# Optimization experiments

Hardware: AMD Instinct MI355X
Metric: run time of the kernel (lower is better)

The kernel has to match this reference:

```python
import jax, jax.numpy as jnp
import numpy as np
import math

B, S, D = 2, 2048, 1024
H, KV, HD = 16, 4, 64
N_REP = H // KV
ROPE_THETA = 1.0e6


def _rope_tables(seq_len, head_dim, theta):
    inv_freq = 1.0 / (theta ** (np.arange(0, head_dim, 2, dtype=np.float32) / head_dim))
    t = np.arange(seq_len, dtype=np.float32)
    freqs = np.outer(t, inv_freq)                      # [S, HD/2]
    emb = np.concatenate([freqs, freqs], axis=-1)      # [S, HD]
    return jnp.asarray(np.cos(emb)), jnp.asarray(np.sin(emb))


def setup_inputs() -> dict:
    key = jax.random.key(0)
    ks = jax.random.split(key, 6)
    cos, sin = _rope_tables(S, HD, ROPE_THETA)
    scale = 0.02
    return {
        "x": jax.random.normal(ks[0], (B, S, D), dtype=jnp.float32),
        "cos": cos,
        "sin": sin,
        "Wq": jax.random.normal(ks[1], (D, H * HD), dtype=jnp.float32) * scale,
        "Wk": jax.random.normal(ks[2], (D, KV * HD), dtype=jnp.float32) * scale,
        "Wv": jax.random.normal(ks[3], (D, KV * HD), dtype=jnp.float32) * scale,
        "Wo": jax.random.normal(ks[4], (H * HD, D), dtype=jnp.float32) * scale,
    }


def _rotate_half(u):
    u1, u2 = u[..., : HD // 2], u[..., HD // 2 :]
    return jnp.concatenate([-u2, u1], axis=-1)


def reference(x, cos, sin, Wq, Wk, Wv, Wo):
    bsz, seq_len, _ = x.shape
    q = (x @ Wq).reshape(bsz, seq_len, H, HD)   # [B,S,H,HD]
    k = (x @ Wk).reshape(bsz, seq_len, KV, HD)  # [B,S,KV,HD]
    v = (x @ Wv).reshape(bsz, seq_len, KV, HD)

    # RoPE: cos/sin [S,HD] broadcast over batch and heads (unsqueeze_dim=1)
    c = cos[:seq_len][None, :, None, :]
    s = sin[:seq_len][None, :, None, :]
    q = q * c + _rotate_half(q) * s
    k = k * c + _rotate_half(k) * s

    # repeat_kv: expand KV heads groupwise to H heads
    k = jnp.repeat(k, N_REP, axis=2)  # [B,S,H,HD]
    v = jnp.repeat(v, N_REP, axis=2)

    q = q.transpose(0, 2, 1, 3)  # [B,H,S,HD]
    k = k.transpose(0, 2, 1, 3)
    v = v.transpose(0, 2, 1, 3)

    scores = jnp.einsum("bhqd,bhkd->bhqk", q, k) / math.sqrt(HD)
    causal = jnp.tril(jnp.ones((seq_len, seq_len), dtype=bool))
    scores = jnp.where(causal[None, None], scores, jnp.finfo(jnp.float32).min)
    probs = jax.nn.softmax(scores.astype(jnp.float32), axis=-1).astype(x.dtype)

    out = jnp.einsum("bhqk,bhkd->bhqd", probs, v)        # [B,H,S,HD]
    out = out.transpose(0, 2, 1, 3).reshape(bsz, seq_len, H * HD)
    return out @ Wo
```

## Files before the change

### kernel.cpp

```cpp
#include <hip/hip_runtime.h>

#define SS 2048
#define NH 16
#define NKV 4
#define HD 64

typedef __bf16 bf16;
typedef __bf16 bf16x4 __attribute__((ext_vector_type(4)));
typedef __bf16 bf16x8 __attribute__((ext_vector_type(8)));
typedef float f32x4 __attribute__((ext_vector_type(4)));

#define SM_SCALE 0.18033688011f

__device__ __forceinline__ void gl_lds16(const bf16* g, bf16* l) {
    __builtin_amdgcn_global_load_lds((const __attribute__((address_space(1))) void*)g,
                                     (__attribute__((address_space(3))) void*)l, 16, 0, 0);
}

__global__ __launch_bounds__(256) void prep_kernel(
    const float* __restrict__ x,
    const float* __restrict__ Wq, const float* __restrict__ Wk,
    const float* __restrict__ Wv, const float* __restrict__ Wo,
    bf16* __restrict__ wqkv_t, bf16* __restrict__ wo_t, bf16* __restrict__ xb)
{
    const int blk = blockIdx.x;
    const int tid = threadIdx.x;
    if (blk >= 640) {
        const size_t i0 = (size_t)(blk - 640) * 16384;
        #pragma unroll
        for (int i = 0; i < 16; ++i) {
            const size_t idx = i0 + i * 1024 + tid * 4;
            const float4 v = *(const float4*)&x[idx];
            bf16x4 o4;
            o4[0] = (bf16)v.x; o4[1] = (bf16)v.y; o4[2] = (bf16)v.z; o4[3] = (bf16)v.w;
            *(bf16x4*)&xb[idx] = o4;
        }
        return;
    }
    const float* W; bf16* Wt; int N, n0, k0;
    if (blk < 256)      { W = Wq; Wt = wqkv_t;                       N = 1024; n0 = (blk & 15) * 64;         k0 = (blk >> 4) * 64; }
    else if (blk < 320) { W = Wk; Wt = wqkv_t + (size_t)1024 * 1024; N = 256;  n0 = ((blk - 256) & 3) * 64;  k0 = ((blk - 256) >> 2) * 64; }
    else if (blk < 384) { W = Wv; Wt = wqkv_t + (size_t)1280 * 1024; N = 256;  n0 = ((blk - 320) & 3) * 64;  k0 = ((blk - 320) >> 2) * 64; }
    else                { W = Wo; Wt = wo_t;                         N = 1024; n0 = ((blk - 384) & 15) * 64; k0 = ((blk - 384) >> 4) * 64; }

    __shared__ float Ts[64][65];
    const int c = tid & 63, rr = tid >> 6;
    #pragma unroll
    for (int i = 0; i < 16; ++i) {
        const int kk = i * 4 + rr;
        Ts[kk][c] = W[(size_t)(k0 + kk) * N + n0 + c];
    }
    __syncthreads();
    #pragma unroll
    for (int i = 0; i < 16; ++i) {
        const int nn = i * 4 + rr;
        Wt[(size_t)(n0 + nn) * 1024 + k0 + c] = (bf16)Ts[c][nn];
    }
}

template<int EPI>
__global__ __launch_bounds__(256) void gemm_bt_kernel(
    const bf16* __restrict__ A, const bf16* __restrict__ Bt, float* __restrict__ C,
    const float* __restrict__ cosp, const float* __restrict__ sinp,
    bf16* __restrict__ qo, bf16* __restrict__ ko, bf16* __restrict__ vto,
    int N, int K, int CB)
{
    __shared__ bf16 As[2][128 * 64];
    __shared__ bf16 Bs[2][128 * 64];
    const int bid = blockIdx.x;
    const int j = bid >> 3;
    const int rb = (bid & 7) + 8 * (j / CB);
    const int cb = j % CB;
    const int m0 = rb * 128, n0 = cb * 128;
    const int tid = threadIdx.x;
    const int w = tid >> 6, lane = tid & 63, g = lane >> 4, li = lane & 15;
    const int wm = w >> 1, wn = w & 1;

    f32x4 acc[4][4];
    const f32x4 z = {0.f, 0.f, 0.f, 0.f};
    #pragma unroll
    for (int i = 0; i < 4; ++i)
        #pragma unroll
        for (int jj = 0; jj < 4; ++jj) acc[i][jj] = z;

    const int srow = tid >> 3;
    const int schunk = ((tid & 7) ^ (srow & 7)) * 8;
    const bf16* pA[4];
    const bf16* pB[4];
    #pragma unroll
    for (int s = 0; s < 4; ++s) {
        pA[s] = A  + (size_t)(m0 + s * 32 + srow) * K + schunk;
        pB[s] = Bt + (size_t)(n0 + s * 32 + srow) * K + schunk;
    }
    const int lw = w * 512;

    const int NT = K >> 6;

    #pragma unroll
    for (int s = 0; s < 4; ++s) gl_lds16(pA[s], &As[0][s * 2048 + lw]);
    #pragma unroll
    for (int s = 0; s < 4; ++s) gl_lds16(pB[s], &Bs[0][s * 2048 + lw]);
    __syncthreads();

    for (int t = 0; t < NT; ++t) {
        const int cur = t & 1;
        const int kk = (t + 1) << 6;
        if (t + 1 < NT) {
            #pragma unroll
            for (int s = 0; s < 4; ++s) gl_lds16(pA[s] + kk, &As[cur ^ 1][s * 2048 + lw]);
            #pragma unroll
            for (int s = 0; s < 4; ++s) gl_lds16(pB[s] + kk, &Bs[cur ^ 1][s * 2048 + lw]);
        }
        #pragma unroll
        for (int tt = 0; tt < 2; ++tt) {
            const int phys = ((tt * 4 + g) ^ (li & 7)) * 8;
            bf16x8 af[4], bfr[4];
            #pragma unroll
            for (int mi = 0; mi < 4; ++mi) af[mi] = *(const bf16x8*)&As[cur][(wm * 64 + mi * 16 + li) * 64 + phys];
            #pragma unroll
            for (int ni = 0; ni < 4; ++ni) bfr[ni] = *(const bf16x8*)&Bs[cur][(wn * 64 + ni * 16 + li) * 64 + phys];
            #pragma unroll
            for (int mi = 0; mi < 4; ++mi)
                #pragma unroll
                for (int ni = 0; ni < 4; ++ni)
                    acc[mi][ni] = __builtin_amdgcn_mfma_f32_16x16x32_bf16(af[mi], bfr[ni], acc[mi][ni], 0, 0, 0);
        }
        __syncthreads();
    }

    const int row0 = m0 + wm * 64, col0 = n0 + wn * 64;
    if (EPI == 0) {
        #pragma unroll
        for (int mi = 0; mi < 4; ++mi)
            #pragma unroll
            for (int ni = 0; ni < 4; ++ni)
                #pragma unroll
                for (int r = 0; r < 4; ++r)
                    C[(size_t)(row0 + mi * 16 + g * 4 + r) * N + col0 + ni * 16 + li] = acc[mi][ni][r];
    } else {
        #pragma unroll
        for (int ni = 0; ni < 4; ++ni) {
            const int col = col0 + ni * 16 + li;
            const int d = col & 63;
            #pragma unroll
            for (int mi = 0; mi < 4; ++mi) {
                #pragma unroll
                for (int r = 0; r < 4; ++r) {
                    const int row = row0 + mi * 16 + g * 4 + r;
                    const int bb = row >> 11, s = row & 2047;
                    float val = acc[mi][ni][r];
                    if (col < 1280) {
                        const float pairv = acc[mi][ni ^ 2][r];
                        const float rot = (d < 32) ? -pairv : pairv;
                        val = val * cosp[s * 64 + d] + rot * sinp[s * 64 + d];
                    }
                    if (col < 1024) {
                        const int hh = col >> 6;
                        qo[(((size_t)bb * NH + hh) * SS + s) * HD + d] = (bf16)(val * SM_SCALE);
                    } else if (col < 1280) {
                        const int kh = (col - 1024) >> 6;
                        ko[(((size_t)bb * NKV + kh) * SS + s) * HD + d] = (bf16)val;
                    } else {
                        const int kh = (col - 1280) >> 6;
                        vto[(((size_t)bb * NKV + kh) * HD + d) * SS + s] = (bf16)val;
                    }
                }
            }
        }
    }
}

__global__ __launch_bounds__(256) void flash_kernel(const bf16* __restrict__ q, const bf16* __restrict__ k,
                                                    const bf16* __restrict__ vt, bf16* __restrict__ o)
{
    __shared__ bf16 Ks[128 * 64];
    __shared__ bf16 Vt[64 * 128];
    __shared__ bf16 Ps[4][16 * 64];

    const int blk = blockIdx.x;
    const int qt = 31 - (blk >> 5);
    const int h = blk & 15;
    const int b = (blk >> 4) & 1;
    const int kvh = h >> 2;
    const int tid = threadIdx.x;
    const int w = tid >> 6, lane = tid & 63, g = lane >> 4, li = lane & 15;

    const bf16* qh = q + ((size_t)b * NH + h) * SS * HD;
    const bf16* kh = k + ((size_t)b * NKV + kvh) * SS * HD;
    const bf16* vh = vt + ((size_t)b * NKV + kvh) * (size_t)HD * SS;

    bf16x8 ones;
    #pragma unroll
    for (int jj = 0; jj < 8; ++jj) ones[jj] = (bf16)1.0f;
    const f32x4 z = {0.f, 0.f, 0.f, 0.f};

    const bf16* qrow = qh + (size_t)(qt * 64 + w * 16 + li) * HD;
    bf16x8 qf[2];
    qf[0] = *(const bf16x8*)(qrow + g * 8);
    qf[1] = *(const bf16x8*)(qrow + 32 + g * 8);

    const int ksrow = tid >> 3;
    const int kchunk = ((tid & 7) ^ (ksrow & 7)) * 8;
    const int vsrow = tid >> 4;
    const int vchunk = (((tid & 15) ^ (vsrow & 7)) & 15) * 8;
    bf16* lK = Ks + (size_t)w * 512;
    bf16* lV = Vt + (size_t)w * 512;

    const int xm = (li & 7) << 1;

    f32x4 o_acc[4], l_acc;
    #pragma unroll
    for (int nt = 0; nt < 4; ++nt) o_acc[nt] = z;
    l_acc = z;

    for (int kt0 = 0; kt0 <= qt; kt0 += 2) {
        __syncthreads();
        {
            #pragma unroll
            for (int s = 0; s < 4; ++s)
                gl_lds16(kh + (size_t)(kt0 * 64 + s * 32 + ksrow) * HD + kchunk, lK + s * 2048);
            #pragma unroll
            for (int s = 0; s < 4; ++s)
                gl_lds16(vh + (size_t)(s * 16 + vsrow) * SS + kt0 * 64 + vchunk, lV + s * 2048);
        }
        __syncthreads();

        #pragma unroll
        for (int sub = 0; sub < 2; ++sub) {
            const int kt = kt0 + sub;
            if (kt > qt) break;

            f32x4 s_acc[4];
            #pragma unroll
            for (int nt = 0; nt < 4; ++nt) s_acc[nt] = z;
            #pragma unroll
            for (int t = 0; t < 2; ++t)
                #pragma unroll
                for (int nt = 0; nt < 4; ++nt) {
                    const bf16x8 kf = *(const bf16x8*)&Ks[(sub * 64 + nt * 16 + li) * 64 + (((t * 4 + g) ^ (li & 7)) * 8)];
                    s_acc[nt] = __builtin_amdgcn_mfma_f32_16x16x32_bf16(kf, qf[t], s_acc[nt], 0, 0, 0);
                }

            if (kt == qt) {
                const int qrow_in = w * 16 + li;
                #pragma unroll
                for (int nt = 0; nt < 4; ++nt) {
                    bf16x4 p4;
                    #pragma unroll
                    for (int r = 0; r < 4; ++r) {
                        float sv = s_acc[nt][r];
                        if (nt * 16 + g * 4 + r > qrow_in) sv = -1e30f;
                        p4[r] = (bf16)exp2f(sv);
                    }
                    *(bf16x4*)&Ps[w][li * 64 + (((nt * 4 + g) ^ xm) * 4)] = p4;
                }
            } else {
                #pragma unroll
                for (int nt = 0; nt < 4; ++nt) {
                    bf16x4 p4;
                    #pragma unroll
                    for (int r = 0; r < 4; ++r) p4[r] = (bf16)exp2f(s_acc[nt][r]);
                    *(bf16x4*)&Ps[w][li * 64 + (((nt * 4 + g) ^ xm) * 4)] = p4;
                }
            }

            #pragma unroll
            for (int t = 0; t < 2; ++t) {
                const bf16x8 pf = *(const bf16x8*)&Ps[w][li * 64 + (((t * 8 + g * 2) ^ xm) * 4)];
                l_acc = __builtin_amdgcn_mfma_f32_16x16x32_bf16(pf, ones, l_acc, 0, 0, 0);
                #pragma unroll
                for (int nt = 0; nt < 4; ++nt) {
                    const bf16x8 vf = *(const bf16x8*)&Vt[(nt * 16 + li) * 128 + (((sub * 8 + t * 4 + g) ^ (li & 7)) * 8)];
                    o_acc[nt] = __builtin_amdgcn_mfma_f32_16x16x32_bf16(pf, vf, o_acc[nt], 0, 0, 0);
                }
            }
        }
    }

    #pragma unroll
    for (int r = 0; r < 4; ++r) {
        const float inv = 1.f / l_acc[r];
        const int s = qt * 64 + w * 16 + g * 4 + r;
        bf16* orow = o + (((size_t)b * SS + s) * NH + h) * HD;
        #pragma unroll
        for (int nt = 0; nt < 4; ++nt) orow[nt * 16 + li] = (bf16)(o_acc[nt][r] * inv);
    }
}

extern "C" void kernel_launch(void* const* d_in, const int* in_sizes, int n_in,
                              void* d_out, int out_size, void* d_ws, size_t ws_size,
                              hipStream_t stream) {
    const float* x     = (const float*)d_in[0];
    const float* cos_t = (const float*)d_in[1];
    const float* sin_t = (const float*)d_in[2];
    const float* Wq    = (const float*)d_in[3];
    const float* Wk    = (const float*)d_in[4];
    const float* Wv    = (const float*)d_in[5];
    const float* Wo    = (const float*)d_in[6];
    float* out = (float*)d_out;

    char* wsb = (char*)d_ws;
    bf16* o_b    = (bf16*)(wsb);
    bf16* wqkv_t = (bf16*)(wsb + 8388608);
    bf16* wo_t   = (bf16*)(wsb + 11534336);
    bf16* q_b    = (bf16*)(wsb + 13631488);
    bf16* k_b    = (bf16*)(wsb + 22020096);
    bf16* vt_b   = (bf16*)(wsb + 24117248);
    bf16* x_b    = (bf16*)(wsb + 26214400);

    prep_kernel<<<896, 256, 0, stream>>>(x, Wq, Wk, Wv, Wo, wqkv_t, wo_t, x_b);

    gemm_bt_kernel<2><<<384, 256, 0, stream>>>(x_b, wqkv_t, nullptr, cos_t, sin_t,
                                               q_b, k_b, vt_b, 1536, 1024, 12);
    flash_kernel<<<1024, 256, 0, stream>>>(q_b, k_b, vt_b, o_b);
    gemm_bt_kernel<0><<<256, 256, 0, stream>>>(o_b, wo_t, out, nullptr, nullptr,
                                               nullptr, nullptr, nullptr, 1024, 1024, 8);
}
```

Before: 177.2 us.

## Deepen async LDS prefetch pipelines in GEMM and flash kernels; widen GEMM to 512 threads

The GEMM now runs 8 waves per block, each computing a 32x64 sub-tile, and keeps two K-tiles in flight. Synchronisation uses explicit vmcnt waits plus raw barriers, and s_setprio raises priority around the MFMA bursts. The flash kernel drops its two-tile staging with full __syncthreads and instead double-buffers 64-key K/V tiles, issuing the next-but-one tile's loads after each compute step. The goal is to hide global-to-LDS latency behind MFMA work and raise occupancy. In exchange the vmcnt counting becomes fragile, and the flash loop does more barriers per unit of work.

```diff
diff --git a/kernel.cpp b/kernel.cpp
--- a/kernel.cpp
+++ b/kernel.cpp
@@ -59,7 +59,7 @@
 }
 
 template<int EPI>
-__global__ __launch_bounds__(256) void gemm_bt_kernel(
+__global__ __launch_bounds__(512) void gemm_bt_kernel(
     const bf16* __restrict__ A, const bf16* __restrict__ Bt, float* __restrict__ C,
     const float* __restrict__ cosp, const float* __restrict__ sinp,
     bf16* __restrict__ qo, bf16* __restrict__ ko, bf16* __restrict__ vto,
@@ -76,62 +76,70 @@
     const int w = tid >> 6, lane = tid & 63, g = lane >> 4, li = lane & 15;
     const int wm = w >> 1, wn = w & 1;
 
-    f32x4 acc[4][4];
+    f32x4 acc[2][4];
     const f32x4 z = {0.f, 0.f, 0.f, 0.f};
     #pragma unroll
-    for (int i = 0; i < 4; ++i)
+    for (int i = 0; i < 2; ++i)
         #pragma unroll
         for (int jj = 0; jj < 4; ++jj) acc[i][jj] = z;
 
     const int srow = tid >> 3;
     const int schunk = ((tid & 7) ^ (srow & 7)) * 8;
-    const bf16* pA[4];
-    const bf16* pB[4];
-    #pragma unroll
-    for (int s = 0; s < 4; ++s) {
-        pA[s] = A  + (size_t)(m0 + s * 32 + srow) * K + schunk;
-        pB[s] = Bt + (size_t)(n0 + s * 32 + srow) * K + schunk;
+    const bf16* pA[2];
+    const bf16* pB[2];
+    #pragma unroll
+    for (int s = 0; s < 2; ++s) {
+        pA[s] = A  + (size_t)(m0 + s * 64 + srow) * K + schunk;
+        pB[s] = Bt + (size_t)(n0 + s * 64 + srow) * K + schunk;
     }
     const int lw = w * 512;
 
     const int NT = K >> 6;
 
     #pragma unroll
-    for (int s = 0; s < 4; ++s) gl_lds16(pA[s], &As[0][s * 2048 + lw]);
-    #pragma unroll
-    for (int s = 0; s < 4; ++s) gl_lds16(pB[s], &Bs[0][s * 2048 + lw]);
-    __syncthreads();
+    for (int s = 0; s < 2; ++s) gl_lds16(pA[s], &As[0][s * 4096 + lw]);
+    #pragma unroll
+    for (int s = 0; s < 2; ++s) gl_lds16(pB[s], &Bs[0][s * 4096 + lw]);
+    #pragma unroll
+    for (int s = 0; s < 2; ++s) gl_lds16(pA[s] + 64, &As[1][s * 4096 + lw]);
+    #pragma unroll
+    for (int s = 0; s < 2; ++s) gl_lds16(pB[s] + 64, &Bs[1][s * 4096 + lw]);
 
     for (int t = 0; t < NT; ++t) {
         const int cur = t & 1;
-        const int kk = (t + 1) << 6;
-        if (t + 1 < NT) {
-            #pragma unroll
-            for (int s = 0; s < 4; ++s) gl_lds16(pA[s] + kk, &As[cur ^ 1][s * 2048 + lw]);
-            #pragma unroll
-            for (int s = 0; s < 4; ++s) gl_lds16(pB[s] + kk, &Bs[cur ^ 1][s * 2048 + lw]);
-        }
+        if (t + 1 < NT) { asm volatile("s_waitcnt vmcnt(4)" ::: "memory"); }
+        else            { asm volatile("s_waitcnt vmcnt(0)" ::: "memory"); }
+        __builtin_amdgcn_s_barrier();
         #pragma unroll
         for (int tt = 0; tt < 2; ++tt) {
             const int phys = ((tt * 4 + g) ^ (li & 7)) * 8;
-            bf16x8 af[4], bfr[4];
-            #pragma unroll
-            for (int mi = 0; mi < 4; ++mi) af[mi] = *(const bf16x8*)&As[cur][(wm * 64 + mi * 16 + li) * 64 + phys];
+            bf16x8 af[2], bfr[4];
+            #pragma unroll
+            for (int mi = 0; mi < 2; ++mi) af[mi] = *(const bf16x8*)&As[cur][(wm * 32 + mi * 16 + li) * 64 + phys];
             #pragma unroll
             for (int ni = 0; ni < 4; ++ni) bfr[ni] = *(const bf16x8*)&Bs[cur][(wn * 64 + ni * 16 + li) * 64 + phys];
-            #pragma unroll
-            for (int mi = 0; mi < 4; ++mi)
+            __builtin_amdgcn_s_setprio(1);
+            #pragma unroll
+            for (int mi = 0; mi < 2; ++mi)
                 #pragma unroll
                 for (int ni = 0; ni < 4; ++ni)
                     acc[mi][ni] = __builtin_amdgcn_mfma_f32_16x16x32_bf16(af[mi], bfr[ni], acc[mi][ni], 0, 0, 0);
-        }
-        __syncthreads();
-    }
-
-    const int row0 = m0 + wm * 64, col0 = n0 + wn * 64;
+            __builtin_amdgcn_s_setprio(0);
+        }
+        __builtin_amdgcn_s_barrier();
+        if (t + 2 < NT) {
+            const int kk = (t + 2) << 6;
+            #pragma unroll
+            for (int s = 0; s < 2; ++s) gl_lds16(pA[s] + kk, &As[cur][s * 4096 + lw]);
+            #pragma unroll
+            for (int s = 0; s < 2; ++s) gl_lds16(pB[s] + kk, &Bs[cur][s * 4096 + lw]);
+        }
+    }
+
+    const int row0 = m0 + wm * 32, col0 = n0 + wn * 64;
     if (EPI == 0) {
         #pragma unroll
-        for (int mi = 0; mi < 4; ++mi)
+        for (int mi = 0; mi < 2; ++mi)
             #pragma unroll
             for (int ni = 0; ni < 4; ++ni)
                 #pragma unroll
@@ -143,7 +151,7 @@
             const int col = col0 + ni * 16 + li;
             const int d = col & 63;
             #pragma unroll
-            for (int mi = 0; mi < 4; ++mi) {
+            for (int mi = 0; mi < 2; ++mi) {
                 #pragma unroll
                 for (int r = 0; r < 4; ++r) {
                     const int row = row0 + mi * 16 + g * 4 + r;
@@ -173,8 +181,8 @@
 __global__ __launch_bounds__(256) void flash_kernel(const bf16* __restrict__ q, const bf16* __restrict__ k,
                                                     const bf16* __restrict__ vt, bf16* __restrict__ o)
 {
-    __shared__ bf16 Ks[128 * 64];
-    __shared__ bf16 Vt[64 * 128];
+    __shared__ bf16 Ks[2][64 * 64];
+    __shared__ bf16 Vt[2][64 * 64];
     __shared__ bf16 Ps[4][16 * 64];
 
     const int blk = blockIdx.x;
@@ -199,12 +207,9 @@
     qf[0] = *(const bf16x8*)(qrow + g * 8);
     qf[1] = *(const bf16x8*)(qrow + 32 + g * 8);
 
-    const int ksrow = tid >> 3;
-    const int kchunk = ((tid & 7) ^ (ksrow & 7)) * 8;
-    const int vsrow = tid >> 4;
-    const int vchunk = (((tid & 15) ^ (vsrow & 7)) & 15) * 8;
-    bf16* lK = Ks + (size_t)w * 512;
-    bf16* lV = Vt + (size_t)w * 512;
+    const int srow = tid >> 3;
+    const int schunk = ((tid & 7) ^ (srow & 7)) * 8;
+    const int lw = w * 512;
 
     const int xm = (li & 7) << 1;
 
@@ -213,67 +218,85 @@
     for (int nt = 0; nt < 4; ++nt) o_acc[nt] = z;
     l_acc = z;
 
-    for (int kt0 = 0; kt0 <= qt; kt0 += 2) {
-        __syncthreads();
-        {
-            #pragma unroll
-            for (int s = 0; s < 4; ++s)
-                gl_lds16(kh + (size_t)(kt0 * 64 + s * 32 + ksrow) * HD + kchunk, lK + s * 2048);
-            #pragma unroll
-            for (int s = 0; s < 4; ++s)
-                gl_lds16(vh + (size_t)(s * 16 + vsrow) * SS + kt0 * 64 + vchunk, lV + s * 2048);
-        }
-        __syncthreads();
-
-        #pragma unroll
-        for (int sub = 0; sub < 2; ++sub) {
-            const int kt = kt0 + sub;
-            if (kt > qt) break;
-
-            f32x4 s_acc[4];
-            #pragma unroll
-            for (int nt = 0; nt < 4; ++nt) s_acc[nt] = z;
-            #pragma unroll
-            for (int t = 0; t < 2; ++t)
-                #pragma unroll
-                for (int nt = 0; nt < 4; ++nt) {
-                    const bf16x8 kf = *(const bf16x8*)&Ks[(sub * 64 + nt * 16 + li) * 64 + (((t * 4 + g) ^ (li & 7)) * 8)];
-                    s_acc[nt] = __builtin_amdgcn_mfma_f32_16x16x32_bf16(kf, qf[t], s_acc[nt], 0, 0, 0);
+    #pragma unroll
+    for (int s = 0; s < 2; ++s)
+        gl_lds16(kh + (size_t)(s * 32 + srow) * HD + schunk, &Ks[0][s * 2048 + lw]);
+    #pragma unroll
+    for (int s = 0; s < 2; ++s)
+        gl_lds16(vh + (size_t)(s * 32 + srow) * SS + schunk, &Vt[0][s * 2048 + lw]);
+    if (qt >= 1) {
+        #pragma unroll
+        for (int s = 0; s < 2; ++s)
+            gl_lds16(kh + (size_t)(64 + s * 32 + srow) * HD + schunk, &Ks[1][s * 2048 + lw]);
+        #pragma unroll
+        for (int s = 0; s < 2; ++s)
+            gl_lds16(vh + (size_t)(s * 32 + srow) * SS + 64 + schunk, &Vt[1][s * 2048 + lw]);
+    }
+
+    for (int kt = 0; kt <= qt; ++kt) {
+        const int cur = kt & 1;
+        if (kt < qt) { asm volatile("s_waitcnt vmcnt(4)" ::: "memory"); }
+        else         { asm volatile("s_waitcnt vmcnt(0)" ::: "memory"); }
+        __builtin_amdgcn_s_barrier();
+
+        f32x4 s_acc[4];
+        #pragma unroll
+        for (int nt = 0; nt < 4; ++nt) s_acc[nt] = z;
+        __builtin_amdgcn_s_setprio(1);
+        #pragma unroll
+        for (int t = 0; t < 2; ++t)
+            #pragma unroll
+            for (int nt = 0; nt < 4; ++nt) {
+                const bf16x8 kf = *(const bf16x8*)&Ks[cur][(nt * 16 + li) * 64 + (((t * 4 + g) ^ (li & 7)) * 8)];
+                s_acc[nt] = __builtin_amdgcn_mfma_f32_16x16x32_bf16(kf, qf[t], s_acc[nt], 0, 0, 0);
+            }
+        __builtin_amdgcn_s_setprio(0);
+
+        if (kt == qt) {
+            const int qrow_in = w * 16 + li;
+            #pragma unroll
+            for (int nt = 0; nt < 4; ++nt) {
+                bf16x4 p4;
+                #pragma unroll
+                for (int r = 0; r < 4; ++r) {
+                    float sv = s_acc[nt][r];
+                    if (nt * 16 + g * 4 + r > qrow_in) sv = -1e30f;
+                    p4[r] = (bf16)exp2f(sv);
                 }
-
-            if (kt == qt) {
-                const int qrow_in = w * 16 + li;
-                #pragma unroll
-                for (int nt = 0; nt < 4; ++nt) {
-                    bf16x4 p4;
-                    #pragma unroll
-                    for (int r = 0; r < 4; ++r) {
-                        float sv = s_acc[nt][r];
-                        if (nt * 16 + g * 4 + r > qrow_in) sv = -1e30f;
-                        p4[r] = (bf16)exp2f(sv);
-                    }
-                    *(bf16x4*)&Ps[w][li * 64 + (((nt * 4 + g) ^ xm) * 4)] = p4;
-                }
-            } else {
-                #pragma unroll
-                for (int nt = 0; nt < 4; ++nt) {
-                    bf16x4 p4;
-                    #pragma unroll
-                    for (int r = 0; r < 4; ++r) p4[r] = (bf16)exp2f(s_acc[nt][r]);
-                    *(bf16x4*)&Ps[w][li * 64 + (((nt * 4 + g) ^ xm) * 4)] = p4;
-                }
-            }
-
-            #pragma unroll
-            for (int t = 0; t < 2; ++t) {
-                const bf16x8 pf = *(const bf16x8*)&Ps[w][li * 64 + (((t * 8 + g * 2) ^ xm) * 4)];
-                l_acc = __builtin_amdgcn_mfma_f32_16x16x32_bf16(pf, ones, l_acc, 0, 0, 0);
-                #pragma unroll
-                for (int nt = 0; nt < 4; ++nt) {
-                    const bf16x8 vf = *(const bf16x8*)&Vt[(nt * 16 + li) * 128 + (((sub * 8 + t * 4 + g) ^ (li & 7)) * 8)];
-                    o_acc[nt] = __builtin_amdgcn_mfma_f32_16x16x32_bf16(pf, vf, o_acc[nt], 0, 0, 0);
-                }
-            }
+                *(bf16x4*)&Ps[w][li * 64 + (((nt * 4 + g) ^ xm) * 4)] = p4;
+            }
+        } else {
+            #pragma unroll
+            for (int nt = 0; nt < 4; ++nt) {
+                bf16x4 p4;
+                #pragma unroll
+                for (int r = 0; r < 4; ++r) p4[r] = (bf16)exp2f(s_acc[nt][r]);
+                *(bf16x4*)&Ps[w][li * 64 + (((nt * 4 + g) ^ xm) * 4)] = p4;
+            }
+        }
+
+        __builtin_amdgcn_s_setprio(1);
+        #pragma unroll
+        for (int t = 0; t < 2; ++t) {
+            const bf16x8 pf = *(const bf16x8*)&Ps[w][li * 64 + (((t * 8 + g * 2) ^ xm) * 4)];
+            l_acc = __builtin_amdgcn_mfma_f32_16x16x32_bf16(pf, ones, l_acc, 0, 0, 0);
+            #pragma unroll
+            for (int nt = 0; nt < 4; ++nt) {
+                const bf16x8 vf = *(const bf16x8*)&Vt[cur][(nt * 16 + li) * 64 + (((t * 4 + g) ^ (li & 7)) * 8)];
+                o_acc[nt] = __builtin_amdgcn_mfma_f32_16x16x32_bf16(pf, vf, o_acc[nt], 0, 0, 0);
+            }
+        }
+        __builtin_amdgcn_s_setprio(0);
+
+        __builtin_amdgcn_s_barrier();
+        if (kt + 2 <= qt) {
+            const size_t kq = (size_t)(kt + 2) * 64;
+            #pragma unroll
+            for (int s = 0; s < 2; ++s)
+                gl_lds16(kh + (kq + s * 32 + srow) * HD + schunk, &Ks[cur][s * 2048 + lw]);
+            #pragma unroll
+            for (int s = 0; s < 2; ++s)
+                gl_lds16(vh + (size_t)(s * 32 + srow) * SS + kq + schunk, &Vt[cur][s * 2048 + lw]);
         }
     }
 
@@ -310,9 +333,9 @@
 
     prep_kernel<<<896, 256, 0, stream>>>(x, Wq, Wk, Wv, Wo, wqkv_t, wo_t, x_b);
 
-    gemm_bt_kernel<2><<<384, 256, 0, stream>>>(x_b, wqkv_t, nullptr, cos_t, sin_t,
+    gemm_bt_kernel<2><<<384, 512, 0, stream>>>(x_b, wqkv_t, nullptr, cos_t, sin_t,
                                                q_b, k_b, vt_b, 1536, 1024, 12);
     flash_kernel<<<1024, 256, 0, stream>>>(q_b, k_b, vt_b, o_b);
-    gemm_bt_kernel<0><<<256, 256, 0, stream>>>(o_b, wo_t, out, nullptr, nullptr,
+    gemm_bt_kernel<0><<<256, 512, 0, stream>>>(o_b, wo_t, out, nullptr, nullptr,
                                                nullptr, nullptr, nullptr, 1024, 1024, 8);
 }
```

Measured after the change: 168.7 us. 1.05x faster.
